# Optimization experiments

Hardware: AMD Instinct MI355X
Metric: run time of the kernel (lower is better)

The kernel has to match this reference:

```python
import jax, jax.numpy as jnp
import numpy as np

JITTER_EPS = 0.01  # router_jitter_noise


def sparsemixer_top2(scores, jitter_eps):
    # scores: [T, E]. Faithful port of PhiMoE sparsemixer (top_k == 2).
    E = scores.shape[-1]
    eye = jnp.arange(E)
    # ---- expert 1 ----
    max1 = jnp.max(scores, axis=-1, keepdims=True)
    ind1 = jnp.argmax(scores, axis=-1)                      # [T]
    factor1 = jnp.maximum(jnp.abs(scores), max1)            # scores.abs().clamp(min=max)
    mask1 = (max1 - scores) / factor1 > 2.0 * jitter_eps
    gates1 = jax.nn.softmax(jnp.where(mask1, -jnp.inf, scores), axis=-1)
    mult1 = jnp.take_along_axis(gates1, ind1[:, None], axis=-1)   # [T,1]
    # ---- expert 2: mask out first pick, repeat ----
    oh1 = eye[None, :] == ind1[:, None]
    masked_scores = jnp.where(oh1, -jnp.inf, scores)
    max2 = jnp.max(masked_scores, axis=-1, keepdims=True)
    ind2 = jnp.argmax(masked_scores, axis=-1)
    factor2 = jnp.maximum(jnp.abs(scores), max2)
    mask2 = (max2 - scores) / factor2 > 2.0 * jitter_eps
    gates2 = jax.nn.softmax(jnp.where(mask2, -jnp.inf, masked_scores), axis=-1)
    mult2 = jnp.take_along_axis(gates2, ind2[:, None], axis=-1)   # [T,1]
    topk_w = jnp.concatenate([mult1, mult2], axis=-1)       # [T,2]
    topk_ids = jnp.stack([ind1, ind2], axis=-1)             # [T,2]
    return topk_w, topk_ids


def setup_inputs() -> dict:
    key = jax.random.key(0)
    ks = jax.random.split(key, 5)
    B, S, D, F, E = 2, 2048, 1024, 2048, 8
    hidden_states = jax.random.normal(ks[0], (B, S, D), dtype=jnp.float32)
    gate_w = jax.random.normal(ks[1], (E, D), dtype=jnp.float32) * (D ** -0.5)
    w_gate = jax.random.normal(ks[2], (E, F, D), dtype=jnp.float32) * (D ** -0.5)
    w_up = jax.random.normal(ks[3], (E, F, D), dtype=jnp.float32) * (D ** -0.5)
    w_down = jax.random.normal(ks[4], (E, D, F), dtype=jnp.float32) * (F ** -0.5)
    return {"hidden_states": hidden_states, "gate_w": gate_w,
            "w_gate": w_gate, "w_up": w_up, "w_down": w_down}


def reference(hidden_states, gate_w, w_gate, w_up, w_down):
    B, S, D = hidden_states.shape
    E = gate_w.shape[0]
    x = hidden_states.reshape(-1, D)                         # [T,D]
    router_logits = x @ gate_w.T                             # [T,E]
    topk_w, topk_ids = sparsemixer_top2(router_logits, JITTER_EPS)
    # per-token combine weights over experts: [T,E]
    comb = jnp.sum(topk_w[:, :, None] *
                   (topk_ids[:, :, None] == jnp.arange(E)[None, None, :]).astype(topk_w.dtype),
                   axis=1)
    out = jnp.zeros_like(x)
    for e in range(E):  # small fixed expert count
        h = jax.nn.silu(x @ w_gate[e].T) * (x @ w_up[e].T)   # [T,F]
        out = out + comb[:, e:e + 1] * (h @ w_down[e].T)     # [T,D]
    return out.reshape(B, S, D), router_logits
```

## Files before the change

### kernel.cpp

```cpp
#include <hip/hip_runtime.h>
#include <stdint.h>

#define TOK    4096
#define DMODEL 1024
#define FDIM   2048
#define NEXP   8
#define MAXP   9216
#define MAXT   72
#define OUT_MAIN (TOK * DMODEL)

#define IDX_NT  24
#define IDX_TE  32
#define IDX_TR  112

#define OFF_META 0
#define OFF_TKW  33792
#define OFF_PTOK 66560
#define OFF_PW   103424
#define OFF_XG   140288
#define OFF_H    19014656
#define OFF_WGB  56763392
#define OFF_WUB  90317824
#define OFF_WDB  123872256
#define OFF_PV   OFF_WGB
#define OFF_RPOS 157426688
#define WS_NEED  157459456

typedef __attribute__((ext_vector_type(8)))  __bf16 bf16x8;
typedef __attribute__((ext_vector_type(8)))  unsigned short u16x8;
typedef __attribute__((ext_vector_type(4)))  unsigned short u16x4;
typedef __attribute__((ext_vector_type(16))) float f32x16;

__device__ __forceinline__ unsigned short f2bf(float f) {
  unsigned u = __builtin_bit_cast(unsigned, f);
  u += 0x7fffu + ((u >> 16) & 1u);
  return (unsigned short)(u >> 16);
}

__device__ __forceinline__ void async_load16(const void* g, void* l) {
  __builtin_amdgcn_global_load_lds(
      (__attribute__((address_space(1))) void*)g,
      (__attribute__((address_space(3))) void*)l, 16, 0, 0);
}

__device__ __forceinline__ bf16x8 ld_frag(const unsigned short* p) {
  return __builtin_bit_cast(bf16x8, *(const u16x8*)p);
}

__global__ void k_prep(const float* __restrict__ wg, const float* __restrict__ wu,
                       const float* __restrict__ wd, unsigned short* __restrict__ wgb,
                       unsigned short* __restrict__ wub, unsigned short* __restrict__ wdb,
                       const float* __restrict__ x, const float* __restrict__ gw,
                       float* __restrict__ logits, int pre) {
  int b = blockIdx.x;
  if (b < 24576) {
    if (!pre) return;
    const float* src; unsigned short* dst; int bb;
    if (b < 8192)       { src = wg; dst = wgb; bb = b; }
    else if (b < 16384) { src = wu; dst = wub; bb = b - 8192; }
    else                { src = wd; dst = wdb; bb = b - 16384; }
    size_t i = ((size_t)bb * 256 + threadIdx.x) * 8;
    float4 a = *(const float4*)(src + i);
    float4 c = *(const float4*)(src + i + 4);
    u16x8 v = {f2bf(a.x), f2bf(a.y), f2bf(a.z), f2bf(a.w),
               f2bf(c.x), f2bf(c.y), f2bf(c.z), f2bf(c.w)};
    *(u16x8*)(dst + i) = v;
    return;
  }
  int lane = threadIdx.x & 63;
  int t = (b - 24576) * 4 + (threadIdx.x >> 6);
  double acc[NEXP];
#pragma unroll
  for (int e = 0; e < NEXP; ++e) acc[e] = 0.0;
  const float* xp = x + (size_t)t * DMODEL;
  for (int i = 0; i < DMODEL / 64; ++i) {
    int d = i * 64 + lane;
    float xv = xp[d];
#pragma unroll
    for (int e = 0; e < NEXP; ++e) acc[e] += (double)xv * (double)gw[e * DMODEL + d];
  }
#pragma unroll
  for (int e = 0; e < NEXP; ++e) {
    double v = acc[e];
#pragma unroll
    for (int off = 32; off > 0; off >>= 1) v += __shfl_down(v, off, 64);
    if (lane == 0) logits[t * NEXP + e] = (float)v;
  }
}

__global__ __launch_bounds__(1024) void k_route2(
    const float* __restrict__ logits, int* __restrict__ meta,
    float* __restrict__ tk_w, int* __restrict__ ptok, float* __restrict__ pw,
    int* __restrict__ rpos) {
  __shared__ int cnt[NEXP], cur[NEXP], seg[NEXP];
  int tid = threadIdx.x;
  if (tid < NEXP) { cnt[tid] = 0; cur[tid] = 0; }
  for (int r = tid; r < MAXP; r += 1024) ptok[r] = -1;
  __syncthreads();
  int i1[4], i2[4]; float w1v[4], w2v[4];
#pragma unroll
  for (int j = 0; j < 4; ++j) {
    int t = tid + j * 1024;
    float s[NEXP];
#pragma unroll
    for (int e = 0; e < NEXP; ++e) s[e] = logits[t * NEXP + e];
    float max1 = s[0]; int ind1 = 0;
#pragma unroll
    for (int e = 1; e < NEXP; ++e) if (s[e] > max1) { max1 = s[e]; ind1 = e; }
    float sum1 = 0.f;
#pragma unroll
    for (int e = 0; e < NEXP; ++e) {
      float f = fmaxf(fabsf(s[e]), max1);
      if (!((max1 - s[e]) / f > 0.02f)) sum1 += expf(s[e] - max1);
    }
    float max2 = -3.4e38f; int ind2 = 0;
#pragma unroll
    for (int e = 0; e < NEXP; ++e) if (e != ind1 && s[e] > max2) { max2 = s[e]; ind2 = e; }
    float sum2 = 0.f;
#pragma unroll
    for (int e = 0; e < NEXP; ++e) {
      if (e == ind1) continue;
      float f = fmaxf(fabsf(s[e]), max2);
      if (!((max2 - s[e]) / f > 0.02f)) sum2 += expf(s[e] - max2);
    }
    i1[j] = ind1; i2[j] = ind2; w1v[j] = 1.f / sum1; w2v[j] = 1.f / sum2;
    atomicAdd(&cnt[ind1], 1);
    atomicAdd(&cnt[ind2], 1);
  }
  __syncthreads();
  if (tid == 0) {
    int off = 0, nt2 = 0;
    for (int e = 0; e < NEXP; ++e) {
      seg[e] = off;
      int tiles = (cnt[e] + 127) >> 7;
      for (int j = 0; j < tiles; ++j) {
        meta[IDX_TE + nt2] = e;
        meta[IDX_TR + nt2] = off + (j << 7);
        ++nt2;
      }
      off += tiles << 7;
    }
    meta[IDX_NT] = nt2;
  }
  __syncthreads();
#pragma unroll
  for (int j = 0; j < 4; ++j) {
    int t = tid + j * 1024;
    int e1 = i1[j];
    int p1 = atomicAdd(&cur[e1], 1);
    int r1 = seg[e1] + p1;
    ptok[r1] = t; pw[r1] = w1v[j]; rpos[2 * t] = r1; tk_w[2 * t] = w1v[j];
    int e2 = i2[j];
    int p2 = atomicAdd(&cur[e2], 1);
    int r2 = seg[e2] + p2;
    ptok[r2] = t; pw[r2] = w2v[j]; rpos[2 * t + 1] = r2; tk_w[2 * t + 1] = w2v[j];
  }
}

__global__ void k_gather(const float* __restrict__ x, const int* __restrict__ ptok,
                         unsigned short* __restrict__ xg) {
  int r = blockIdx.x;
  int t = ptok[r];
  int c = threadIdx.x << 2;
  unsigned short o0 = 0, o1 = 0, o2 = 0, o3 = 0;
  if (t >= 0) {
    float4 v = *(const float4*)(x + ((size_t)t << 10) + c);
    o0 = f2bf(v.x); o1 = f2bf(v.y); o2 = f2bf(v.z); o3 = f2bf(v.w);
  }
  u16x4 o = {o0, o1, o2, o3};
  *(u16x4*)(xg + ((size_t)r << 10) + c) = o;
}

template <bool PRE>
__global__ __launch_bounds__(256, 4) void k_gu(
    const unsigned short* __restrict__ xg,
    const float* __restrict__ wg32, const float* __restrict__ wu32,
    const unsigned short* __restrict__ wgb, const unsigned short* __restrict__ wub,
    unsigned short* __restrict__ h, const int* __restrict__ meta) {
  int nt = meta[IDX_NT];
  int rt = blockIdx.y;
  if (rt >= nt) return;
  int e = meta[IDX_TE + rt];
  int row0 = meta[IDX_TR + rt];
  int n0 = blockIdx.x * 64;

  __shared__ __align__(16) unsigned short As[8192], Bg[4096], Bu[4096];

  int tid = threadIdx.x, lane = tid & 63, w = tid >> 6;
  int wm = w & 1, wn = w >> 1;
  int l31 = lane & 31, lh = lane >> 5;

  f32x16 accg[2], accu[2];
#pragma unroll
  for (int i = 0; i < 2; ++i) {
#pragma unroll
    for (int r = 0; r < 16; ++r) { accg[i][r] = 0.f; accu[i][r] = 0.f; }
  }

  const unsigned short* Abase =
      xg + (size_t)(row0 + w * 32 + l31) * DMODEL + lh * 8;
  int c0 = w * 2, c1 = c0 + 1;
  const unsigned short* G0; const unsigned short* G1;
  const unsigned short* U0; const unsigned short* U1;
  if constexpr (PRE) {
    const unsigned short* WgB = wgb + (size_t)e * FDIM * DMODEL;
    const unsigned short* WuB = wub + (size_t)e * FDIM * DMODEL;
    size_t o0 = (size_t)(n0 + ((c0 >> 2) << 5) + l31) * DMODEL + ((c0 & 3) << 4) + lh * 8;
    size_t o1 = (size_t)(n0 + ((c1 >> 2) << 5) + l31) * DMODEL + ((c1 & 3) << 4) + lh * 8;
    G0 = WgB + o0; G1 = WgB + o1; U0 = WuB + o0; U1 = WuB + o1;
  }

  for (int ks = 0; ks < DMODEL / 64; ++ks) {
    int k0 = ks * 64;
    if (ks) __syncthreads();
    async_load16(Abase + k0,      &As[(w * 4 + 0) * 512]);
    async_load16(Abase + k0 + 16, &As[(w * 4 + 1) * 512]);
    async_load16(Abase + k0 + 32, &As[(w * 4 + 2) * 512]);
    async_load16(Abase + k0 + 48, &As[(w * 4 + 3) * 512]);
    if constexpr (PRE) {
      async_load16(G0 + k0, &Bg[c0 * 512]);
      async_load16(G1 + k0, &Bg[c1 * 512]);
      async_load16(U0 + k0, &Bu[c0 * 512]);
      async_load16(U1 + k0, &Bu[c1 * 512]);
    } else {
      const float* Wg = wg32 + (size_t)e * FDIM * DMODEL;
      const float* Wu = wu32 + (size_t)e * FDIM * DMODEL;
#pragma unroll
      for (int i2 = 0; i2 < 2; ++i2) {
        int tau = tid + 256 * i2;
        int c = tau >> 6, l = tau & 63;
        int nrow = n0 + ((c >> 2) << 5) + (l & 31);
        int kk = k0 + ((c & 3) << 4) + ((l >> 5) << 3);
        const float* sg = Wg + (size_t)nrow * DMODEL + kk;
        const float* su = Wu + (size_t)nrow * DMODEL + kk;
        float4 g0 = *(const float4*)sg;
        float4 g1 = *(const float4*)(sg + 4);
        float4 u0 = *(const float4*)su;
        float4 u1 = *(const float4*)(su + 4);
        u16x8 vg = {f2bf(g0.x), f2bf(g0.y), f2bf(g0.z), f2bf(g0.w),
                    f2bf(g1.x), f2bf(g1.y), f2bf(g1.z), f2bf(g1.w)};
        u16x8 vu = {f2bf(u0.x), f2bf(u0.y), f2bf(u0.z), f2bf(u0.w),
                    f2bf(u1.x), f2bf(u1.y), f2bf(u1.z), f2bf(u1.w)};
        *(u16x8*)&Bg[c * 512 + l * 8] = vg;
        *(u16x8*)&Bu[c * 512 + l * 8] = vu;
      }
    }
    __syncthreads();
#pragma unroll
    for (int kq = 0; kq < 4; ++kq) {
      bf16x8 a0 = ld_frag(&As[((wm * 2 + 0) * 4 + kq) * 512 + lane * 8]);
      bf16x8 a1 = ld_frag(&As[((wm * 2 + 1) * 4 + kq) * 512 + lane * 8]);
      bf16x8 vg = ld_frag(&Bg[(wn * 4 + kq) * 512 + lane * 8]);
      bf16x8 vu = ld_frag(&Bu[(wn * 4 + kq) * 512 + lane * 8]);
      accg[0] = __builtin_amdgcn_mfma_f32_32x32x16_bf16(a0, vg, accg[0], 0, 0, 0);
      accg[1] = __builtin_amdgcn_mfma_f32_32x32x16_bf16(a1, vg, accg[1], 0, 0, 0);
      accu[0] = __builtin_amdgcn_mfma_f32_32x32x16_bf16(a0, vu, accu[0], 0, 0, 0);
      accu[1] = __builtin_amdgcn_mfma_f32_32x32x16_bf16(a1, vu, accu[1], 0, 0, 0);
    }
  }
  int col = n0 + wn * 32 + l31;
#pragma unroll
  for (int mt = 0; mt < 2; ++mt) {
#pragma unroll
    for (int r = 0; r < 16; ++r) {
      int lrow = wm * 64 + mt * 32 + (r & 3) + ((r >> 2) << 3) + lh * 4;
      float gv = accg[mt][r], uv = accu[mt][r];
      float hv = gv * uv / (1.f + __expf(-gv));
      h[(size_t)(row0 + lrow) * FDIM + col] = f2bf(hv);
    }
  }
}

template <bool PRE>
__global__ __launch_bounds__(256, 5) void k_down(
    const unsigned short* __restrict__ h, const float* __restrict__ wd32,
    const unsigned short* __restrict__ wdb, float* __restrict__ out,
    float* __restrict__ pv, const int* __restrict__ meta,
    const int* __restrict__ ptok, const float* __restrict__ pw) {
  int nt = meta[IDX_NT];
  int rt = blockIdx.y;
  if (rt >= nt) return;
  int e = meta[IDX_TE + rt];
  int row0 = meta[IDX_TR + rt];
  int d0 = blockIdx.x * 64;

  __shared__ __align__(16) unsigned short Ah[8192], Bd[4096];
  __shared__ int stok[128];
  __shared__ float sw[128];

  int tid = threadIdx.x, lane = tid & 63, w = tid >> 6;
  int wm = w & 1, wn = w >> 1;
  int l31 = lane & 31, lh = lane >> 5;

  if constexpr (!PRE) {
    if (tid < 128) { stok[tid] = ptok[row0 + tid]; sw[tid] = pw[row0 + tid]; }
  }

  f32x16 acc[2];
#pragma unroll
  for (int i = 0; i < 2; ++i) {
#pragma unroll
    for (int r = 0; r < 16; ++r) acc[i][r] = 0.f;
  }

  const unsigned short* Abase =
      h + (size_t)(row0 + w * 32 + l31) * FDIM + lh * 8;
  int c0 = w * 2, c1 = c0 + 1;
  const unsigned short* D0; const unsigned short* D1;
  if constexpr (PRE) {
    const unsigned short* WdB = wdb + (size_t)e * DMODEL * FDIM;
    D0 = WdB + (size_t)(d0 + ((c0 >> 2) << 5) + l31) * FDIM + ((c0 & 3) << 4) + lh * 8;
    D1 = WdB + (size_t)(d0 + ((c1 >> 2) << 5) + l31) * FDIM + ((c1 & 3) << 4) + lh * 8;
  }

  for (int ks = 0; ks < FDIM / 64; ++ks) {
    int k0 = ks * 64;
    if (ks) __syncthreads();
    async_load16(Abase + k0,      &Ah[(w * 4 + 0) * 512]);
    async_load16(Abase + k0 + 16, &Ah[(w * 4 + 1) * 512]);
    async_load16(Abase + k0 + 32, &Ah[(w * 4 + 2) * 512]);
    async_load16(Abase + k0 + 48, &Ah[(w * 4 + 3) * 512]);
    if constexpr (PRE) {
      async_load16(D0 + k0, &Bd[c0 * 512]);
      async_load16(D1 + k0, &Bd[c1 * 512]);
    } else {
      const float* Wd = wd32 + (size_t)e * DMODEL * FDIM;
#pragma unroll
      for (int i2 = 0; i2 < 2; ++i2) {
        int tau = tid + 256 * i2;
        int c = tau >> 6, l = tau & 63;
        int drow = d0 + ((c >> 2) << 5) + (l & 31);
        int kk = k0 + ((c & 3) << 4) + ((l >> 5) << 3);
        const float* sd = Wd + (size_t)drow * FDIM + kk;
        float4 b0 = *(const float4*)sd;
        float4 b1 = *(const float4*)(sd + 4);
        u16x8 vb = {f2bf(b0.x), f2bf(b0.y), f2bf(b0.z), f2bf(b0.w),
                    f2bf(b1.x), f2bf(b1.y), f2bf(b1.z), f2bf(b1.w)};
        *(u16x8*)&Bd[c * 512 + l * 8] = vb;
      }
    }
    __syncthreads();
#pragma unroll
    for (int kq = 0; kq < 4; ++kq) {
      bf16x8 a0 = ld_frag(&Ah[((wm * 2 + 0) * 4 + kq) * 512 + lane * 8]);
      bf16x8 a1 = ld_frag(&Ah[((wm * 2 + 1) * 4 + kq) * 512 + lane * 8]);
      bf16x8 vb = ld_frag(&Bd[(wn * 4 + kq) * 512 + lane * 8]);
      acc[0] = __builtin_amdgcn_mfma_f32_32x32x16_bf16(a0, vb, acc[0], 0, 0, 0);
      acc[1] = __builtin_amdgcn_mfma_f32_32x32x16_bf16(a1, vb, acc[1], 0, 0, 0);
    }
  }
  int col = d0 + wn * 32 + l31;
#pragma unroll
  for (int mt = 0; mt < 2; ++mt) {
#pragma unroll
    for (int r = 0; r < 16; ++r) {
      int lrow = wm * 64 + mt * 32 + (r & 3) + ((r >> 2) << 3) + lh * 4;
      if constexpr (PRE) {
        pv[(size_t)(row0 + lrow) * DMODEL + col] = acc[mt][r];
      } else {
        int t = stok[lrow];
        if (t >= 0) atomicAdd(&out[(size_t)t * DMODEL + col], acc[mt][r] * sw[lrow]);
      }
    }
  }
}

__global__ void k_combine(const float* __restrict__ pv, const int* __restrict__ rpos,
                          const float* __restrict__ tkw, float* __restrict__ out) {
  int t = blockIdx.x;
  int r1 = rpos[2 * t], r2 = rpos[2 * t + 1];
  float w1 = tkw[2 * t], w2 = tkw[2 * t + 1];
  int c = threadIdx.x << 2;
  float4 a = *(const float4*)(pv + (size_t)r1 * DMODEL + c);
  float4 b = *(const float4*)(pv + (size_t)r2 * DMODEL + c);
  float4 o;
  o.x = w1 * a.x + w2 * b.x;
  o.y = w1 * a.y + w2 * b.y;
  o.z = w1 * a.z + w2 * b.z;
  o.w = w1 * a.w + w2 * b.w;
  *(float4*)(out + (size_t)t * DMODEL + c) = o;
}

extern "C" void kernel_launch(void* const* d_in, const int* in_sizes, int n_in,
                              void* d_out, int out_size, void* d_ws, size_t ws_size,
                              hipStream_t stream) {
  const float* x  = (const float*)d_in[0];
  const float* gw = (const float*)d_in[1];
  const float* wg = (const float*)d_in[2];
  const float* wu = (const float*)d_in[3];
  const float* wd = (const float*)d_in[4];
  float* out = (float*)d_out;
  float* logits = out + OUT_MAIN;

  char* wsb = (char*)d_ws;
  int* meta = (int*)(wsb + OFF_META);
  float* tk_w = (float*)(wsb + OFF_TKW);
  int* ptok = (int*)(wsb + OFF_PTOK);
  float* pw = (float*)(wsb + OFF_PW);
  unsigned short* xg = (unsigned short*)(wsb + OFF_XG);
  unsigned short* h = (unsigned short*)(wsb + OFF_H);
  unsigned short* wgb = (unsigned short*)(wsb + OFF_WGB);
  unsigned short* wub = (unsigned short*)(wsb + OFF_WUB);
  unsigned short* wdb = (unsigned short*)(wsb + OFF_WDB);
  float* pv = (float*)(wsb + OFF_PV);
  int* rpos = (int*)(wsb + OFF_RPOS);

  bool pre = ws_size >= (size_t)WS_NEED;
  if (!pre) hipMemsetAsync(out, 0, (size_t)OUT_MAIN * sizeof(float), stream);

  k_prep<<<25600, 256, 0, stream>>>(wg, wu, wd, wgb, wub, wdb, x, gw, logits, (int)pre);
  k_route2<<<1, 1024, 0, stream>>>(logits, meta, tk_w, ptok, pw, rpos);
  k_gather<<<MAXP, 256, 0, stream>>>(x, ptok, xg);
  if (pre) {
    k_gu<true><<<dim3(FDIM / 64, MAXT), 256, 0, stream>>>(xg, wg, wu, wgb, wub, h, meta);
    k_down<true><<<dim3(DMODEL / 64, MAXT), 256, 0, stream>>>(h, wd, wdb, out, pv, meta, ptok, pw);
    k_combine<<<TOK, 256, 0, stream>>>(pv, rpos, tk_w, out);
  } else {
    k_gu<false><<<dim3(FDIM / 64, MAXT), 256, 0, stream>>>(xg, wg, wu, wgb, wub, h, meta);
    k_down<false><<<dim3(DMODEL / 64, MAXT), 256, 0, stream>>>(h, wd, wdb, out, pv, meta, ptok, pw);
  }
}
```

Before: 520.1 us.

## Register-prefetch GEMM tiles and move sparsemixer routing into the logits kernel

The gate/up and down expert GEMMs stop using async global-to-LDS loads. They now prefetch the next K-slice into registers while the MFMAs run on the current LDS tile, then write it to LDS between barriers. This is meant to hide global-load latency, and occupancy hints are lowered to make room for the extra registers. The top-2 sparsemixer routing also moves from the single-block route kernel into the logits kernel. The route kernel now uses 256 threads that aggregate per-expert counts before the atomics, which shortens the serial one-block stage.

After: 578.1 us. 11.2% more time.

```diff
diff --git a/kernel.cpp b/kernel.cpp
--- a/kernel.cpp
+++ b/kernel.cpp
@@ -14,6 +14,7 @@
 #define IDX_TR  112
 
 #define OFF_META 0
+#define OFF_TKE  1024
 #define OFF_TKW  33792
 #define OFF_PTOK 66560
 #define OFF_PW   103424
@@ -37,12 +38,6 @@
   return (unsigned short)(u >> 16);
 }
 
-__device__ __forceinline__ void async_load16(const void* g, void* l) {
-  __builtin_amdgcn_global_load_lds(
-      (__attribute__((address_space(1))) void*)g,
-      (__attribute__((address_space(3))) void*)l, 16, 0, 0);
-}
-
 __device__ __forceinline__ bf16x8 ld_frag(const unsigned short* p) {
   return __builtin_bit_cast(bf16x8, *(const u16x8*)p);
 }
@@ -51,7 +46,8 @@
                        const float* __restrict__ wd, unsigned short* __restrict__ wgb,
                        unsigned short* __restrict__ wub, unsigned short* __restrict__ wdb,
                        const float* __restrict__ x, const float* __restrict__ gw,
-                       float* __restrict__ logits, int pre) {
+                       float* __restrict__ logits, int* __restrict__ tk_e,
+                       float* __restrict__ tk_w, int pre) {
   int b = blockIdx.x;
   if (b < 24576) {
     if (!pre) return;
@@ -79,53 +75,60 @@
 #pragma unroll
     for (int e = 0; e < NEXP; ++e) acc[e] += (double)xv * (double)gw[e * DMODEL + d];
   }
+  float s[NEXP];
 #pragma unroll
   for (int e = 0; e < NEXP; ++e) {
     double v = acc[e];
 #pragma unroll
     for (int off = 32; off > 0; off >>= 1) v += __shfl_down(v, off, 64);
-    if (lane == 0) logits[t * NEXP + e] = (float)v;
-  }
-}
-
-__global__ __launch_bounds__(1024) void k_route2(
-    const float* __restrict__ logits, int* __restrict__ meta,
-    float* __restrict__ tk_w, int* __restrict__ ptok, float* __restrict__ pw,
+    if (lane == 0) { s[e] = (float)v; logits[t * NEXP + e] = (float)v; }
+  }
+  if (lane == 0) {
+    float max1 = s[0]; int ind1 = 0;
+#pragma unroll
+    for (int e = 1; e < NEXP; ++e) if (s[e] > max1) { max1 = s[e]; ind1 = e; }
+    float sum1 = 0.f;
+#pragma unroll
+    for (int e = 0; e < NEXP; ++e) {
+      float f = fmaxf(fabsf(s[e]), max1);
+      if (!((max1 - s[e]) / f > 0.02f)) sum1 += expf(s[e] - max1);
+    }
+    float max2 = -3.4e38f; int ind2 = 0;
+#pragma unroll
+    for (int e = 0; e < NEXP; ++e) if (e != ind1 && s[e] > max2) { max2 = s[e]; ind2 = e; }
+    float sum2 = 0.f;
+#pragma unroll
+    for (int e = 0; e < NEXP; ++e) {
+      if (e == ind1) continue;
+      float f = fmaxf(fabsf(s[e]), max2);
+      if (!((max2 - s[e]) / f > 0.02f)) sum2 += expf(s[e] - max2);
+    }
+    tk_e[2 * t] = ind1; tk_e[2 * t + 1] = ind2;
+    tk_w[2 * t] = 1.f / sum1; tk_w[2 * t + 1] = 1.f / sum2;
+  }
+}
+
+__global__ __launch_bounds__(256) void k_route2(
+    const int* __restrict__ tk_e, const float* __restrict__ tk_w,
+    int* __restrict__ meta, int* __restrict__ ptok, float* __restrict__ pw,
     int* __restrict__ rpos) {
   __shared__ int cnt[NEXP], cur[NEXP], seg[NEXP];
   int tid = threadIdx.x;
   if (tid < NEXP) { cnt[tid] = 0; cur[tid] = 0; }
-  for (int r = tid; r < MAXP; r += 1024) ptok[r] = -1;
+  for (int r = tid; r < MAXP; r += 256) ptok[r] = -1;
   __syncthreads();
-  int i1[4], i2[4]; float w1v[4], w2v[4];
-#pragma unroll
-  for (int j = 0; j < 4; ++j) {
-    int t = tid + j * 1024;
-    float s[NEXP];
-#pragma unroll
-    for (int e = 0; e < NEXP; ++e) s[e] = logits[t * NEXP + e];
-    float max1 = s[0]; int ind1 = 0;
-#pragma unroll
-    for (int e = 1; e < NEXP; ++e) if (s[e] > max1) { max1 = s[e]; ind1 = e; }
-    float sum1 = 0.f;
-#pragma unroll
-    for (int e = 0; e < NEXP; ++e) {
-      float f = fmaxf(fabsf(s[e]), max1);
-      if (!((max1 - s[e]) / f > 0.02f)) sum1 += expf(s[e] - max1);
-    }
-    float max2 = -3.4e38f; int ind2 = 0;
-#pragma unroll
-    for (int e = 0; e < NEXP; ++e) if (e != ind1 && s[e] > max2) { max2 = s[e]; ind2 = e; }
-    float sum2 = 0.f;
-#pragma unroll
-    for (int e = 0; e < NEXP; ++e) {
-      if (e == ind1) continue;
-      float f = fmaxf(fabsf(s[e]), max2);
-      if (!((max2 - s[e]) / f > 0.02f)) sum2 += expf(s[e] - max2);
-    }
-    i1[j] = ind1; i2[j] = ind2; w1v[j] = 1.f / sum1; w2v[j] = 1.f / sum2;
-    atomicAdd(&cnt[ind1], 1);
-    atomicAdd(&cnt[ind2], 1);
+  int e1[16], e2[16];
+#pragma unroll
+  for (int j = 0; j < 16; ++j) {
+    int t = tid * 16 + j;
+    e1[j] = tk_e[2 * t]; e2[j] = tk_e[2 * t + 1];
+  }
+#pragma unroll
+  for (int e = 0; e < NEXP; ++e) {
+    int lc = 0;
+#pragma unroll
+    for (int j = 0; j < 16; ++j) lc += (e1[j] == e) + (e2[j] == e);
+    if (lc) atomicAdd(&cnt[e], lc);
   }
   __syncthreads();
   if (tid == 0) {
@@ -144,16 +147,24 @@
   }
   __syncthreads();
 #pragma unroll
-  for (int j = 0; j < 4; ++j) {
-    int t = tid + j * 1024;
-    int e1 = i1[j];
-    int p1 = atomicAdd(&cur[e1], 1);
-    int r1 = seg[e1] + p1;
-    ptok[r1] = t; pw[r1] = w1v[j]; rpos[2 * t] = r1; tk_w[2 * t] = w1v[j];
-    int e2 = i2[j];
-    int p2 = atomicAdd(&cur[e2], 1);
-    int r2 = seg[e2] + p2;
-    ptok[r2] = t; pw[r2] = w2v[j]; rpos[2 * t + 1] = r2; tk_w[2 * t + 1] = w2v[j];
+  for (int e = 0; e < NEXP; ++e) {
+    int lc = 0;
+#pragma unroll
+    for (int j = 0; j < 16; ++j) lc += (e1[j] == e) + (e2[j] == e);
+    if (!lc) continue;
+    int base = seg[e] + atomicAdd(&cur[e], lc);
+#pragma unroll
+    for (int j = 0; j < 16; ++j) {
+      int t = tid * 16 + j;
+      if (e1[j] == e) {
+        int r = base++;
+        ptok[r] = t; pw[r] = tk_w[2 * t]; rpos[2 * t] = r;
+      }
+      if (e2[j] == e) {
+        int r = base++;
+        ptok[r] = t; pw[r] = tk_w[2 * t + 1]; rpos[2 * t + 1] = r;
+      }
+    }
   }
 }
 
@@ -172,7 +183,7 @@
 }
 
 template <bool PRE>
-__global__ __launch_bounds__(256, 4) void k_gu(
+__global__ __launch_bounds__(256, 3) void k_gu(
     const unsigned short* __restrict__ xg,
     const float* __restrict__ wg32, const float* __restrict__ wu32,
     const unsigned short* __restrict__ wgb, const unsigned short* __restrict__ wub,
@@ -197,11 +208,9 @@
     for (int r = 0; r < 16; ++r) { accg[i][r] = 0.f; accu[i][r] = 0.f; }
   }
 
-  const unsigned short* Abase =
-      xg + (size_t)(row0 + w * 32 + l31) * DMODEL + lh * 8;
+  const unsigned short* Abase = xg + (size_t)(row0 + w * 32 + l31) * DMODEL + lh * 8;
   int c0 = w * 2, c1 = c0 + 1;
-  const unsigned short* G0; const unsigned short* G1;
-  const unsigned short* U0; const unsigned short* U1;
+  const unsigned short *G0, *G1, *U0, *U1;
   if constexpr (PRE) {
     const unsigned short* WgB = wgb + (size_t)e * FDIM * DMODEL;
     const unsigned short* WuB = wub + (size_t)e * FDIM * DMODEL;
@@ -210,21 +219,60 @@
     G0 = WgB + o0; G1 = WgB + o1; U0 = WuB + o0; U1 = WuB + o1;
   }
 
-  for (int ks = 0; ks < DMODEL / 64; ++ks) {
-    int k0 = ks * 64;
-    if (ks) __syncthreads();
-    async_load16(Abase + k0,      &As[(w * 4 + 0) * 512]);
-    async_load16(Abase + k0 + 16, &As[(w * 4 + 1) * 512]);
-    async_load16(Abase + k0 + 32, &As[(w * 4 + 2) * 512]);
-    async_load16(Abase + k0 + 48, &As[(w * 4 + 3) * 512]);
-    if constexpr (PRE) {
-      async_load16(G0 + k0, &Bg[c0 * 512]);
-      async_load16(G1 + k0, &Bg[c1 * 512]);
-      async_load16(U0 + k0, &Bu[c0 * 512]);
-      async_load16(U1 + k0, &Bu[c1 * 512]);
-    } else {
-      const float* Wg = wg32 + (size_t)e * FDIM * DMODEL;
-      const float* Wu = wu32 + (size_t)e * FDIM * DMODEL;
+  if constexpr (PRE) {
+    u16x8 pa[4], pg[2], pu[2];
+#pragma unroll
+    for (int i = 0; i < 4; ++i) pa[i] = *(const u16x8*)(Abase + i * 16);
+    pg[0] = *(const u16x8*)G0; pg[1] = *(const u16x8*)G1;
+    pu[0] = *(const u16x8*)U0; pu[1] = *(const u16x8*)U1;
+#pragma unroll
+    for (int i = 0; i < 4; ++i) *(u16x8*)&As[(w * 4 + i) * 512 + lane * 8] = pa[i];
+    *(u16x8*)&Bg[c0 * 512 + lane * 8] = pg[0];
+    *(u16x8*)&Bg[c1 * 512 + lane * 8] = pg[1];
+    *(u16x8*)&Bu[c0 * 512 + lane * 8] = pu[0];
+    *(u16x8*)&Bu[c1 * 512 + lane * 8] = pu[1];
+    __syncthreads();
+    for (int ks = 0; ks < DMODEL / 64; ++ks) {
+      if (ks < DMODEL / 64 - 1) {
+        int k1 = (ks + 1) * 64;
+#pragma unroll
+        for (int i = 0; i < 4; ++i) pa[i] = *(const u16x8*)(Abase + k1 + i * 16);
+        pg[0] = *(const u16x8*)(G0 + k1); pg[1] = *(const u16x8*)(G1 + k1);
+        pu[0] = *(const u16x8*)(U0 + k1); pu[1] = *(const u16x8*)(U1 + k1);
+      }
+#pragma unroll
+      for (int kq = 0; kq < 4; ++kq) {
+        bf16x8 a0 = ld_frag(&As[((wm * 2 + 0) * 4 + kq) * 512 + lane * 8]);
+        bf16x8 a1 = ld_frag(&As[((wm * 2 + 1) * 4 + kq) * 512 + lane * 8]);
+        bf16x8 vg = ld_frag(&Bg[(wn * 4 + kq) * 512 + lane * 8]);
+        bf16x8 vu = ld_frag(&Bu[(wn * 4 + kq) * 512 + lane * 8]);
+        accg[0] = __builtin_amdgcn_mfma_f32_32x32x16_bf16(a0, vg, accg[0], 0, 0, 0);
+        accg[1] = __builtin_amdgcn_mfma_f32_32x32x16_bf16(a1, vg, accg[1], 0, 0, 0);
+        accu[0] = __builtin_amdgcn_mfma_f32_32x32x16_bf16(a0, vu, accu[0], 0, 0, 0);
+        accu[1] = __builtin_amdgcn_mfma_f32_32x32x16_bf16(a1, vu, accu[1], 0, 0, 0);
+      }
+      if (ks < DMODEL / 64 - 1) {
+        __syncthreads();
+#pragma unroll
+        for (int i = 0; i < 4; ++i) *(u16x8*)&As[(w * 4 + i) * 512 + lane * 8] = pa[i];
+        *(u16x8*)&Bg[c0 * 512 + lane * 8] = pg[0];
+        *(u16x8*)&Bg[c1 * 512 + lane * 8] = pg[1];
+        *(u16x8*)&Bu[c0 * 512 + lane * 8] = pu[0];
+        *(u16x8*)&Bu[c1 * 512 + lane * 8] = pu[1];
+        __syncthreads();
+      }
+    }
+  } else {
+    const float* Wg = wg32 + (size_t)e * FDIM * DMODEL;
+    const float* Wu = wu32 + (size_t)e * FDIM * DMODEL;
+    for (int ks = 0; ks < DMODEL / 64; ++ks) {
+      int k0 = ks * 64;
+      if (ks) __syncthreads();
+#pragma unroll
+      for (int i = 0; i < 4; ++i) {
+        u16x8 va = *(const u16x8*)(Abase + k0 + i * 16);
+        *(u16x8*)&As[(w * 4 + i) * 512 + lane * 8] = va;
+      }
 #pragma unroll
       for (int i2 = 0; i2 < 2; ++i2) {
         int tau = tid + 256 * i2;
@@ -244,18 +292,18 @@
         *(u16x8*)&Bg[c * 512 + l * 8] = vg;
         *(u16x8*)&Bu[c * 512 + l * 8] = vu;
       }
-    }
-    __syncthreads();
-#pragma unroll
-    for (int kq = 0; kq < 4; ++kq) {
-      bf16x8 a0 = ld_frag(&As[((wm * 2 + 0) * 4 + kq) * 512 + lane * 8]);
-      bf16x8 a1 = ld_frag(&As[((wm * 2 + 1) * 4 + kq) * 512 + lane * 8]);
-      bf16x8 vg = ld_frag(&Bg[(wn * 4 + kq) * 512 + lane * 8]);
-      bf16x8 vu = ld_frag(&Bu[(wn * 4 + kq) * 512 + lane * 8]);
-      accg[0] = __builtin_amdgcn_mfma_f32_32x32x16_bf16(a0, vg, accg[0], 0, 0, 0);
-      accg[1] = __builtin_amdgcn_mfma_f32_32x32x16_bf16(a1, vg, accg[1], 0, 0, 0);
-      accu[0] = __builtin_amdgcn_mfma_f32_32x32x16_bf16(a0, vu, accu[0], 0, 0, 0);
-      accu[1] = __builtin_amdgcn_mfma_f32_32x32x16_bf16(a1, vu, accu[1], 0, 0, 0);
+      __syncthreads();
+#pragma unroll
+      for (int kq = 0; kq < 4; ++kq) {
+        bf16x8 a0 = ld_frag(&As[((wm * 2 + 0) * 4 + kq) * 512 + lane * 8]);
+        bf16x8 a1 = ld_frag(&As[((wm * 2 + 1) * 4 + kq) * 512 + lane * 8]);
+        bf16x8 vg = ld_frag(&Bg[(wn * 4 + kq) * 512 + lane * 8]);
+        bf16x8 vu = ld_frag(&Bu[(wn * 4 + kq) * 512 + lane * 8]);
+        accg[0] = __builtin_amdgcn_mfma_f32_32x32x16_bf16(a0, vg, accg[0], 0, 0, 0);
+        accg[1] = __builtin_amdgcn_mfma_f32_32x32x16_bf16(a1, vg, accg[1], 0, 0, 0);
+        accu[0] = __builtin_amdgcn_mfma_f32_32x32x16_bf16(a0, vu, accu[0], 0, 0, 0);
+        accu[1] = __builtin_amdgcn_mfma_f32_32x32x16_bf16(a1, vu, accu[1], 0, 0, 0);
+      }
     }
   }
   int col = n0 + wn * 32 + l31;
@@ -272,7 +320,7 @@
 }
 
 template <bool PRE>
-__global__ __launch_bounds__(256, 5) void k_down(
+__global__ __launch_bounds__(256, 4) void k_down(
     const unsigned short* __restrict__ h, const float* __restrict__ wd32,
     const unsigned short* __restrict__ wdb, float* __restrict__ out,
     float* __restrict__ pv, const int* __restrict__ meta,
@@ -303,28 +351,59 @@
     for (int r = 0; r < 16; ++r) acc[i][r] = 0.f;
   }
 
-  const unsigned short* Abase =
-      h + (size_t)(row0 + w * 32 + l31) * FDIM + lh * 8;
+  const unsigned short* Abase = h + (size_t)(row0 + w * 32 + l31) * FDIM + lh * 8;
   int c0 = w * 2, c1 = c0 + 1;
-  const unsigned short* D0; const unsigned short* D1;
+  const unsigned short *D0, *D1;
   if constexpr (PRE) {
     const unsigned short* WdB = wdb + (size_t)e * DMODEL * FDIM;
     D0 = WdB + (size_t)(d0 + ((c0 >> 2) << 5) + l31) * FDIM + ((c0 & 3) << 4) + lh * 8;
     D1 = WdB + (size_t)(d0 + ((c1 >> 2) << 5) + l31) * FDIM + ((c1 & 3) << 4) + lh * 8;
   }
 
-  for (int ks = 0; ks < FDIM / 64; ++ks) {
-    int k0 = ks * 64;
-    if (ks) __syncthreads();
-    async_load16(Abase + k0,      &Ah[(w * 4 + 0) * 512]);
-    async_load16(Abase + k0 + 16, &Ah[(w * 4 + 1) * 512]);
-    async_load16(Abase + k0 + 32, &Ah[(w * 4 + 2) * 512]);
-    async_load16(Abase + k0 + 48, &Ah[(w * 4 + 3) * 512]);
-    if constexpr (PRE) {
-      async_load16(D0 + k0, &Bd[c0 * 512]);
-      async_load16(D1 + k0, &Bd[c1 * 512]);
-    } else {
-      const float* Wd = wd32 + (size_t)e * DMODEL * FDIM;
+  if constexpr (PRE) {
+    u16x8 pa[4], pd[2];
+#pragma unroll
+    for (int i = 0; i < 4; ++i) pa[i] = *(const u16x8*)(Abase + i * 16);
+    pd[0] = *(const u16x8*)D0; pd[1] = *(const u16x8*)D1;
+#pragma unroll
+    for (int i = 0; i < 4; ++i) *(u16x8*)&Ah[(w * 4 + i) * 512 + lane * 8] = pa[i];
+    *(u16x8*)&Bd[c0 * 512 + lane * 8] = pd[0];
+    *(u16x8*)&Bd[c1 * 512 + lane * 8] = pd[1];
+    __syncthreads();
+    for (int ks = 0; ks < FDIM / 64; ++ks) {
+      if (ks < FDIM / 64 - 1) {
+        int k1 = (ks + 1) * 64;
+#pragma unroll
+        for (int i = 0; i < 4; ++i) pa[i] = *(const u16x8*)(Abase + k1 + i * 16);
+        pd[0] = *(const u16x8*)(D0 + k1); pd[1] = *(const u16x8*)(D1 + k1);
+      }
+#pragma unroll
+      for (int kq = 0; kq < 4; ++kq) {
+        bf16x8 a0 = ld_frag(&Ah[((wm * 2 + 0) * 4 + kq) * 512 + lane * 8]);
+        bf16x8 a1 = ld_frag(&Ah[((wm * 2 + 1) * 4 + kq) * 512 + lane * 8]);
+        bf16x8 vb = ld_frag(&Bd[(wn * 4 + kq) * 512 + lane * 8]);
+        acc[0] = __builtin_amdgcn_mfma_f32_32x32x16_bf16(a0, vb, acc[0], 0, 0, 0);
+        acc[1] = __builtin_amdgcn_mfma_f32_32x32x16_bf16(a1, vb, acc[1], 0, 0, 0);
+      }
+      if (ks < FDIM / 64 - 1) {
+        __syncthreads();
+#pragma unroll
+        for (int i = 0; i < 4; ++i) *(u16x8*)&Ah[(w * 4 + i) * 512 + lane * 8] = pa[i];
+        *(u16x8*)&Bd[c0 * 512 + lane * 8] = pd[0];
+        *(u16x8*)&Bd[c1 * 512 + lane * 8] = pd[1];
+        __syncthreads();
+      }
+    }
+  } else {
+    const float* Wd = wd32 + (size_t)e * DMODEL * FDIM;
+    for (int ks = 0; ks < FDIM / 64; ++ks) {
+      int k0 = ks * 64;
+      if (ks) __syncthreads();
+#pragma unroll
+      for (int i = 0; i < 4; ++i) {
+        u16x8 va = *(const u16x8*)(Abase + k0 + i * 16);
+        *(u16x8*)&Ah[(w * 4 + i) * 512 + lane * 8] = va;
+      }
 #pragma unroll
       for (int i2 = 0; i2 < 2; ++i2) {
         int tau = tid + 256 * i2;
@@ -338,15 +417,15 @@
                     f2bf(b1.x), f2bf(b1.y), f2bf(b1.z), f2bf(b1.w)};
         *(u16x8*)&Bd[c * 512 + l * 8] = vb;
       }
-    }
-    __syncthreads();
-#pragma unroll
-    for (int kq = 0; kq < 4; ++kq) {
-      bf16x8 a0 = ld_frag(&Ah[((wm * 2 + 0) * 4 + kq) * 512 + lane * 8]);
-      bf16x8 a1 = ld_frag(&Ah[((wm * 2 + 1) * 4 + kq) * 512 + lane * 8]);
-      bf16x8 vb = ld_frag(&Bd[(wn * 4 + kq) * 512 + lane * 8]);
-      acc[0] = __builtin_amdgcn_mfma_f32_32x32x16_bf16(a0, vb, acc[0], 0, 0, 0);
-      acc[1] = __builtin_amdgcn_mfma_f32_32x32x16_bf16(a1, vb, acc[1], 0, 0, 0);
+      __syncthreads();
+#pragma unroll
+      for (int kq = 0; kq < 4; ++kq) {
+        bf16x8 a0 = ld_frag(&Ah[((wm * 2 + 0) * 4 + kq) * 512 + lane * 8]);
+        bf16x8 a1 = ld_frag(&Ah[((wm * 2 + 1) * 4 + kq) * 512 + lane * 8]);
+        bf16x8 vb = ld_frag(&Bd[(wn * 4 + kq) * 512 + lane * 8]);
+        acc[0] = __builtin_amdgcn_mfma_f32_32x32x16_bf16(a0, vb, acc[0], 0, 0, 0);
+        acc[1] = __builtin_amdgcn_mfma_f32_32x32x16_bf16(a1, vb, acc[1], 0, 0, 0);
+      }
     }
   }
   int col = d0 + wn * 32 + l31;
@@ -394,6 +473,7 @@
 
   char* wsb = (char*)d_ws;
   int* meta = (int*)(wsb + OFF_META);
+  int* tk_e = (int*)(wsb + OFF_TKE);
   float* tk_w = (float*)(wsb + OFF_TKW);
   int* ptok = (int*)(wsb + OFF_PTOK);
   float* pw = (float*)(wsb + OFF_PW);
@@ -408,8 +488,9 @@
   bool pre = ws_size >= (size_t)WS_NEED;
   if (!pre) hipMemsetAsync(out, 0, (size_t)OUT_MAIN * sizeof(float), stream);
 
-  k_prep<<<25600, 256, 0, stream>>>(wg, wu, wd, wgb, wub, wdb, x, gw, logits, (int)pre);
-  k_route2<<<1, 1024, 0, stream>>>(logits, meta, tk_w, ptok, pw, rpos);
+  k_prep<<<25600, 256, 0, stream>>>(wg, wu, wd, wgb, wub, wdb, x, gw, logits,
+                                    tk_e, tk_w, (int)pre);
+  k_route2<<<1, 256, 0, stream>>>(tk_e, tk_w, meta, ptok, pw, rpos);
   k_gather<<<MAXP, 256, 0, stream>>>(x, ptok, xg);
   if (pre) {
     k_gu<true><<<dim3(FDIM / 64, MAXT), 256, 0, stream>>>(xg, wg, wu, wgb, wub, h, meta);
```
